# Optimization experiments

Hardware: AMD Instinct MI355X
Metric: run time of the kernel (lower is better)

## Reference

```python
import jax, jax.numpy as jnp
import numpy as np

SIDE = 32
N_NODES = SIDE * SIDE          # n_nodes = 1024
WIDTH = 128
IN_DIM = 128
T_DIM = 2
U_DIM = 1
BATCH = 8
MSG_STEPS = int(np.sqrt(N_NODES))  # 32
LN_EPS = 1e-5


def _create_grid():
    # matches GEN.create_grid for t_dim == 2
    pos = np.array([[i / (SIDE - 1), j / (SIDE - 1)]
                    for i in range(SIDE) for j in range(SIDE)], dtype=np.float32)
    edges = []
    for i in range(1, SIDE):
        for j in range(1, SIDE):
            a = SIDE * i + j
            b = SIDE * (i - 1) + j
            c = SIDE * i + (j - 1)
            edges += [[a, b], [b, a], [c, a], [a, c]]
    edge_index = np.array(edges, dtype=np.int64).T  # [2, E]
    return pos, edge_index


def setup_inputs() -> dict:
    key = jax.random.key(0)
    ks = jax.random.split(key, 16)
    node_pos_np, edge_index_np = _create_grid()

    def lin(k, fan_in, fan_out):
        kw, kb = jax.random.split(k)
        bound = 1.0 / np.sqrt(fan_in)
        W = jax.random.uniform(kw, (fan_in, fan_out), jnp.float32, -bound, bound)
        b = jax.random.uniform(kb, (fan_out,), jnp.float32, -bound, bound)
        return W, b

    We1, be1 = lin(ks[0], IN_DIM, WIDTH)
    We2, be2 = lin(ks[1], WIDTH, WIDTH)
    We3, be3 = lin(ks[2], WIDTH, WIDTH)
    Wg, bg = lin(ks[3], WIDTH + T_DIM, WIDTH)
    Wd1, bd1 = lin(ks[4], WIDTH + T_DIM, WIDTH)
    Wd2, bd2 = lin(ks[5], WIDTH, WIDTH)
    Wd3, bd3 = lin(ks[6], WIDTH, U_DIM)

    return {
        'X1': jax.random.uniform(ks[7], (BATCH, IN_DIM + T_DIM), jnp.float32),
        'node_pos': jnp.asarray(node_pos_np),
        'edge_index': jnp.asarray(edge_index_np),
        'We1': We1, 'be1': be1, 'We2': We2, 'be2': be2, 'We3': We3, 'be3': be3,
        'Wg': Wg, 'bg': bg,
        'gamma': jnp.ones((WIDTH,), jnp.float32),
        'beta': jnp.zeros((WIDTH,), jnp.float32),
        'Wd1': Wd1, 'bd1': bd1, 'Wd2': Wd2, 'bd2': bd2, 'Wd3': Wd3, 'bd3': bd3,
    }


def _gen_forward(X1, node_pos, edge_index, We1, be1, We2, be2, We3, be3,
                 Wg, bg, gamma, beta, Wd1, bd1, Wd2, bd2, Wd3, bd3):
    s, t = X1[:, :-T_DIM], X1[:, -T_DIM:]

    # encoder MLP: Linear-ReLU-Linear-ReLU-Linear
    h = jax.nn.relu(s @ We1 + be1)
    h = jax.nn.relu(h @ We2 + be2)
    enc = h @ We3 + be3                                   # [B, W]

    # per-sample graph construction: softmax over node distance to origin
    # (identical for every sample), node_features = weight @ enc[i][None,:]
    d0 = jnp.sqrt(jnp.sum(node_pos ** 2, axis=1, keepdims=True))  # [N,1]
    w0 = jax.nn.softmax(-d0, axis=0)                              # [N,1]
    x = w0[None, :, :] * enc[:, None, :]                          # [B,N,W]

    # GCNConv normalization with added self-loops (symmetric norm)
    row, col = edge_index[0], edge_index[1]
    deg = jnp.ones((N_NODES,), x.dtype).at[col].add(1.0)
    dinv = deg ** -0.5
    enorm = dinv[row] * dinv[col]   # edge norm
    snorm = dinv * dinv             # self-loop norm
    posb = jnp.broadcast_to(node_pos[None], (x.shape[0], N_NODES, T_DIM))

    def step(xc, _):
        xin = jnp.concatenate([posb, xc], axis=-1)        # [B,N,W+2]
        xw = xin @ Wg                                     # [B,N,W]
        msgs = enorm[None, :, None] * xw[:, row, :]       # [B,E,W]
        agg = (snorm[None, :, None] * xw).at[:, col, :].add(msgs) + bg
        xn = xc + agg
        mu = jnp.mean(xn, axis=-1, keepdims=True)
        var = jnp.var(xn, axis=-1, keepdims=True)
        xn = (xn - mu) * jax.lax.rsqrt(var + LN_EPS) * gamma + beta
        return xn, None

    x, _ = jax.lax.scan(step, x, None, length=MSG_STEPS)  # [B,N,W]

    # readout: softmax over node distance to query point t
    dist = jnp.sqrt(jnp.sum((node_pos[None] - t[:, None, :]) ** 2,
                            axis=2, keepdims=True))       # [B,N,1]
    wt = jax.nn.softmax(-dist, axis=1)                    # [B,N,1]
    hidden = jnp.einsum('bnk,bnw->bw', wt, x)             # [B,W]
    hidden = jnp.concatenate([hidden, t], axis=1)

    h = jax.nn.relu(hidden @ Wd1 + bd1)
    h = jax.nn.relu(h @ Wd2 + bd2)
    y = (h @ Wd3 + bd3).squeeze()                         # [B] (u_dim == 1)
    return y


def reference(X1, node_pos, edge_index, We1, be1, We2, be2, We3, be3,
              Wg, bg, gamma, beta, Wd1, bd1, Wd2, bd2, Wd3, bd3):
    return _gen_forward(X1, node_pos, edge_index, We1, be1, We2, be2, We3, be3,
                        Wg, bg, gamma, beta, Wd1, bd1, Wd2, bd2, Wd3, bd3)
```

## Files before the change

kernel.cpp:

```cpp
#include <hip/hip_runtime.h>

#define NODES 1024
#define WD    128
#define NSTEPS 32
#define LNEPS 1e-5f

typedef __bf16 bf16x8 __attribute__((ext_vector_type(8)));
typedef float  f32x4  __attribute__((ext_vector_type(4)));
typedef int    i32x4  __attribute__((ext_vector_type(4)));

__device__ __forceinline__ f32x4 mfma16(i32x4 a, i32x4 b, f32x4 c) {
  return __builtin_amdgcn_mfma_f32_16x16x32_bf16(
      __builtin_bit_cast(bf16x8, a), __builtin_bit_cast(bf16x8, b), c, 0, 0, 0);
}

__device__ __forceinline__ unsigned short f2bf(float f) {
  union { float f; unsigned u; } v; v.f = f;
  unsigned r = v.u + 0x7FFF + ((v.u >> 16) & 1);
  return (unsigned short)(r >> 16);
}
__device__ __forceinline__ float bf2f(unsigned short h) {
  union { unsigned u; float f; } v; v.u = ((unsigned)h) << 16;
  return v.f;
}

__device__ __forceinline__ float dinv_of(int n) {
  const int i = n >> 5, j = n & 31;
  int cnt = 1;
  cnt += (i >= 1 && j >= 1) ? 1 : 0;
  cnt += (i <= 30 && j >= 1) ? 1 : 0;
  cnt += (i >= 1 && j >= 1) ? 1 : 0;
  cnt += (i >= 1 && j <= 30) ? 1 : 0;
  return 1.f / sqrtf((float)cnt);
}

__device__ __forceinline__ void lay512(const float* __restrict__ W,
                                       const float* __restrict__ bias,
                                       const float* __restrict__ src,
                                       float* __restrict__ dst, int tid,
                                       bool relu_) {
  const int c = tid & 127;
  const int b0 = tid >> 7;
  float a0 = bias ? bias[c] : 0.f;
  float a1 = a0;
#pragma unroll 8
  for (int k = 0; k < WD; k++) {
    const float wv = W[k * WD + c];
    a0 += src[b0 * WD + k] * wv;
    a1 += src[(b0 + 4) * WD + k] * wv;
  }
  dst[b0 * WD + c] = relu_ ? fmaxf(a0, 0.f) : a0;
  dst[(b0 + 4) * WD + c] = relu_ ? fmaxf(a1, 0.f) : a1;
  __syncthreads();
}

__global__ __launch_bounds__(512) void init_kernel(
    const float* __restrict__ X1, const float* __restrict__ pos,
    const float* __restrict__ We1, const float* __restrict__ be1,
    const float* __restrict__ We2, const float* __restrict__ be2,
    const float* __restrict__ We3, const float* __restrict__ be3,
    const float* __restrict__ Wg, const float* __restrict__ bg,
    float* __restrict__ X, float* __restrict__ XW0, float* __restrict__ Q,
    int* __restrict__ Bpk) {
  __shared__ float ioA[1024];
  __shared__ float ioB[1024];
  __shared__ float red[512];
  const int tid = threadIdx.x;
  const int v0 = blockIdx.x * 4;
  const float* W2 = Wg + 2 * WD;

  for (int i = tid; i < 1024; i += 512) ioA[i] = X1[(i >> 7) * 130 + (i & 127)];
  __syncthreads();
  lay512(We1, be1, ioA, ioB, tid, true);
  lay512(We2, be2, ioB, ioA, tid, true);
  lay512(We3, be3, ioA, ioB, tid, false);
  lay512(W2, nullptr, ioB, ioA, tid, false);

  {
    float es = 0.f;
#pragma unroll
    for (int r = 0; r < 2; r++) {
      const int n = tid + 512 * r;
      const float px = pos[2 * n], py = pos[2 * n + 1];
      es += expf(-sqrtf(px * px + py * py));
    }
    red[tid] = es;
  }
  __syncthreads();
  for (int s = 256; s > 0; s >>= 1) {
    if (tid < s) red[tid] += red[tid + s];
    __syncthreads();
  }
  const float w0sum = red[0];

  {
    const int lr = tid >> 4, cq = tid & 15, c0 = cq * 8;
    const int b = lr >> 2, nl = lr & 3, v = v0 + nl;
    const int grow = (b << 10) + v;
    const float pxv = pos[2 * v], pyv = pos[2 * v + 1];
    const float w0v = expf(-sqrtf(pxv * pxv + pyv * pyv)) / w0sum;
#pragma unroll
    for (int q4 = 0; q4 < 2; q4++) {
      const float4 e = *(const float4*)(ioB + b * WD + c0 + 4 * q4);
      const float4 e2 = *(const float4*)(ioA + b * WD + c0 + 4 * q4);
      *(float4*)(X + (size_t)grow * WD + c0 + 4 * q4) =
          make_float4(w0v * e.x, w0v * e.y, w0v * e.z, w0v * e.w);
      *(float4*)(XW0 + (size_t)grow * WD + c0 + 4 * q4) =
          make_float4(w0v * e2.x, w0v * e2.y, w0v * e2.z, w0v * e2.w);
    }
  }
  {
    const int vq = v0 + (tid >> 7);
    const int cc = tid & 127;
    const float dv = dinv_of(vq);
    const float dvv = dv * dv;
    const int iv = vq >> 5, jv = vq & 31;
    float cx = dvv * pos[2 * vq], cy = dvv * pos[2 * vq + 1];
    const bool ex[4] = {(iv >= 1) && (jv >= 1), (iv <= 30) && (jv >= 1),
                        (iv >= 1) && (jv >= 1), (iv >= 1) && (jv <= 30)};
    const int du[4] = {-32, 32, -1, 1};
#pragma unroll
    for (int e = 0; e < 4; e++) {
      if (ex[e]) {
        const int u = vq + du[e];
        const float w = dinv_of(u) * dv;
        cx += w * pos[2 * u];
        cy += w * pos[2 * u + 1];
      }
    }
    Q[vq * WD + cc] = bg[cc] + cx * Wg[cc] + cy * Wg[WD + cc];
  }
  if (tid < 64) {
    const int e = blockIdx.x * 64 + tid;
    const int nt = e >> 11, l = (e >> 5) & 63, half = (e >> 4) & 1;
    const int kt = (e >> 2) & 3, d = e & 3;
    const int k0 = 32 * kt + ((l >> 4) << 3) + 2 * d;
    const int n = 16 * nt + (l & 15);
    const float w0_ = W2[k0 * WD + n];
    const float w1_ = W2[(k0 + 1) * WD + n];
    const unsigned short h0 = f2bf(w0_), h1 = f2bf(w1_);
    int val;
    if (half == 0) {
      val = (int)h0 | ((int)h1 << 16);
    } else {
      val = (int)f2bf(w0_ - bf2f(h0)) | ((int)f2bf(w1_ - bf2f(h1)) << 16);
    }
    Bpk[e] = val;
  }
}

__global__ __launch_bounds__(512) void step_kernel(
    float* __restrict__ X, const float* __restrict__ XWin,
    float* __restrict__ XWout, const int* __restrict__ Bpk,
    const float* __restrict__ Q, const float* __restrict__ gamma,
    const float* __restrict__ beta, const int mode) {
  __shared__ int Ah[32 * 68];
  __shared__ int Al[32 * 68];
  const int tid = threadIdx.x;
  const int v0 = blockIdx.x * 4;
  const int wv = tid >> 6, l = tid & 63;

  i32x4 bh[4], bl[4];
  if (mode) {
    const int lb0 = (wv * 64 + l) * 32;
#pragma unroll
    for (int kt = 0; kt < 4; kt++) {
      bh[kt] = *(const i32x4*)(Bpk + lb0 + kt * 4);
      bl[kt] = *(const i32x4*)(Bpk + lb0 + 16 + kt * 4);
    }
  }

  const int lr = tid >> 4, cq = tid & 15, c0 = cq * 8;
  const int b = lr >> 2, nl = lr & 3, v = v0 + nl;
  const int grow = (b << 10) + v;
  const float dv = dinv_of(v);
  const float dvv = dv * dv;
  const int iv = v >> 5, jv = v & 31;
  const bool ex[4] = {(iv >= 1) && (jv >= 1), (iv <= 30) && (jv >= 1),
                      (iv >= 1) && (jv >= 1), (iv >= 1) && (jv <= 30)};
  const int du[4] = {-32, 32, -1, 1};

  float y[8];
  {
    const float* xr = X + (size_t)grow * WD + c0;
    const float* qr = Q + v * WD + c0;
    const float* wr = XWin + (size_t)grow * WD + c0;
#pragma unroll
    for (int q4 = 0; q4 < 2; q4++) {
      const float4 a = *(const float4*)(xr + 4 * q4);
      const float4 qq = *(const float4*)(qr + 4 * q4);
      const float4 w = *(const float4*)(wr + 4 * q4);
      y[4 * q4 + 0] = a.x + qq.x + dvv * w.x;
      y[4 * q4 + 1] = a.y + qq.y + dvv * w.y;
      y[4 * q4 + 2] = a.z + qq.z + dvv * w.z;
      y[4 * q4 + 3] = a.w + qq.w + dvv * w.w;
    }
  }
#pragma unroll
  for (int e = 0; e < 4; e++) {
    const int u = ex[e] ? v + du[e] : v;
    const float w = ex[e] ? dinv_of(u) * dv : 0.f;
    const float* nr = XWin + (size_t)((b << 10) + u) * WD + c0;
#pragma unroll
    for (int q4 = 0; q4 < 2; q4++) {
      const float4 t = *(const float4*)(nr + 4 * q4);
      y[4 * q4 + 0] += w * t.x;
      y[4 * q4 + 1] += w * t.y;
      y[4 * q4 + 2] += w * t.z;
      y[4 * q4 + 3] += w * t.w;
    }
  }
  float s1 = 0.f, s2 = 0.f;
#pragma unroll
  for (int q = 0; q < 8; q++) { s1 += y[q]; s2 += y[q] * y[q]; }
#pragma unroll
  for (int m = 1; m < 16; m <<= 1) {
    s1 += __shfl_xor(s1, m);
    s2 += __shfl_xor(s2, m);
  }
  const float mu = s1 * (1.f / 128.f);
  const float var = s2 * (1.f / 128.f) - mu * mu;
  const float rs = 1.f / sqrtf(var + LNEPS);
  {
    const float* g4 = gamma + c0;
    const float* b4 = beta + c0;
    float* xo = X + (size_t)grow * WD + c0;
    float xn[8];
#pragma unroll
    for (int q = 0; q < 8; q++) xn[q] = (y[q] - mu) * rs * g4[q] + b4[q];
    *(float4*)(xo) = make_float4(xn[0], xn[1], xn[2], xn[3]);
    *(float4*)(xo + 4) = make_float4(xn[4], xn[5], xn[6], xn[7]);
    if (mode) {
      int hw[4], lw[4];
#pragma unroll
      for (int d = 0; d < 4; d++) {
        const unsigned short ha = f2bf(xn[2 * d]);
        const unsigned short hb = f2bf(xn[2 * d + 1]);
        hw[d] = (int)ha | ((int)hb << 16);
        lw[d] = (int)f2bf(xn[2 * d] - bf2f(ha)) |
                ((int)f2bf(xn[2 * d + 1] - bf2f(hb)) << 16);
      }
      const int abase = lr * 68 + cq * 4;
      *(i32x4*)(Ah + abase) = i32x4{hw[0], hw[1], hw[2], hw[3]};
      *(i32x4*)(Al + abase) = i32x4{lw[0], lw[1], lw[2], lw[3]};
    }
  }

  if (mode) {
    __syncthreads();
    const int g4 = (l >> 4) << 2;
    const int mrow0 = (l & 15) * 68;
    const int mrow1 = mrow0 + 16 * 68;
    f32x4 acc[2] = {};
#pragma unroll
    for (int kt = 0; kt < 4; kt++) {
      const int off = 16 * kt + g4;
      const i32x4 ah0 = *(const i32x4*)(Ah + mrow0 + off);
      const i32x4 ah1 = *(const i32x4*)(Ah + mrow1 + off);
      const i32x4 al0 = *(const i32x4*)(Al + mrow0 + off);
      const i32x4 al1 = *(const i32x4*)(Al + mrow1 + off);
      acc[0] = mfma16(ah0, bh[kt], acc[0]);
      acc[1] = mfma16(ah1, bh[kt], acc[1]);
      acc[0] = mfma16(ah0, bl[kt], acc[0]);
      acc[1] = mfma16(ah1, bl[kt], acc[1]);
      acc[0] = mfma16(al0, bh[kt], acc[0]);
      acc[1] = mfma16(al1, bh[kt], acc[1]);
    }
    const int colb = 16 * wv + (l & 15);
    const int rbase = (l >> 4) << 2;
#pragma unroll
    for (int mt = 0; mt < 2; mt++)
#pragma unroll
      for (int r = 0; r < 4; r++) {
        const int lrr = 16 * mt + rbase + r;
        const int gr = ((lrr >> 2) << 10) + v0 + (lrr & 3);
        XWout[(size_t)gr * WD + colb] = acc[mt][r];
      }
  }
}

__global__ __launch_bounds__(1024) void hiddec_kernel(
    const float* __restrict__ pos, const float* __restrict__ X1,
    const float* __restrict__ Xf, const float* __restrict__ Wd1,
    const float* __restrict__ bd1, const float* __restrict__ Wd2,
    const float* __restrict__ bd2, const float* __restrict__ Wd3,
    const float* __restrict__ bd3, float* __restrict__ out) {
  __shared__ float wsh[NODES];
  __shared__ float red[16];
  __shared__ float asum[8][WD];
  __shared__ float hid[132];
  __shared__ float hh[WD];
  const int b = blockIdx.x;
  const int n = threadIdx.x;
  const float tx = X1[b * 130 + 128], ty = X1[b * 130 + 129];
  const float px = pos[2 * n] - tx, py = pos[2 * n + 1] - ty;
  const float e = expf(-sqrtf(px * px + py * py));
  float s = e;
#pragma unroll
  for (int m = 32; m >= 1; m >>= 1) s += __shfl_xor(s, m);
  if ((n & 63) == 0) red[n >> 6] = s;
  __syncthreads();
  float tot = 0.f;
#pragma unroll
  for (int w = 0; w < 16; w++) tot += red[w];
  wsh[n] = e / tot;
  __syncthreads();
  const int c = n & 127, g = n >> 7;
  {
    const float* xp = Xf + ((size_t)b * NODES + g * 128) * WD + c;
    const float* wp = wsh + g * 128;
    float a = 0.f;
#pragma unroll 4
    for (int it = 0; it < 128; it++) a += wp[it] * xp[it * WD];
    asum[g][c] = a;
  }
  __syncthreads();
  if (g == 0) {
    float t2 = asum[0][c];
#pragma unroll
    for (int gg = 1; gg < 8; gg++) t2 += asum[gg][c];
    hid[c] = t2;
  }
  if (n == 0) { hid[128] = tx; hid[129] = ty; }
  __syncthreads();
  float a1v = 0.f;
  if (n < 128) {
    a1v = bd1[n];
    for (int k = 0; k < 130; k++) a1v += hid[k] * Wd1[k * WD + n];
  }
  __syncthreads();
  if (n < 128) hh[n] = fmaxf(a1v, 0.f);
  __syncthreads();
  float p = 0.f;
  if (n < 128) {
    float a2 = bd2[n];
#pragma unroll 8
    for (int k = 0; k < WD; k++) a2 += hh[k] * Wd2[k * WD + n];
    p = fmaxf(a2, 0.f) * Wd3[n];
  }
#pragma unroll
  for (int m = 32; m >= 1; m >>= 1) p += __shfl_xor(p, m);
  if ((n & 63) == 0) red[n >> 6] = p;
  __syncthreads();
  if (n == 0) out[b] = red[0] + red[1] + bd3[0];
}

extern "C" void kernel_launch(void* const* d_in, const int* in_sizes, int n_in,
                              void* d_out, int out_size, void* d_ws,
                              size_t ws_size, hipStream_t stream) {
  const float* X1 = (const float*)d_in[0];
  const float* pos = (const float*)d_in[1];
  const float* We1 = (const float*)d_in[3];
  const float* be1 = (const float*)d_in[4];
  const float* We2 = (const float*)d_in[5];
  const float* be2 = (const float*)d_in[6];
  const float* We3 = (const float*)d_in[7];
  const float* be3 = (const float*)d_in[8];
  const float* Wg = (const float*)d_in[9];
  const float* bg = (const float*)d_in[10];
  const float* gamma = (const float*)d_in[11];
  const float* beta = (const float*)d_in[12];
  const float* Wd1 = (const float*)d_in[13];
  const float* bd1 = (const float*)d_in[14];
  const float* Wd2 = (const float*)d_in[15];
  const float* bd2 = (const float*)d_in[16];
  const float* Wd3 = (const float*)d_in[17];
  const float* bd3 = (const float*)d_in[18];
  float* out = (float*)d_out;
  float* f = (float*)d_ws;

  float* Q = f;
  int* Bpk = (int*)(f + 131072);
  float* X = f + 147456;
  float* XWa = f + 1196032;
  float* XWb = f + 2244608;

  init_kernel<<<256, 512, 0, stream>>>(X1, pos, We1, be1, We2, be2, We3, be3,
                                       Wg, bg, X, XWa, Q, Bpk);
  for (int t = 0; t < NSTEPS; t++) {
    const float* xin = (t & 1) ? XWb : XWa;
    float* xout = (t & 1) ? XWa : XWb;
    step_kernel<<<256, 512, 0, stream>>>(X, xin, xout, Bpk, Q, gamma, beta,
                                         (t < NSTEPS - 1) ? 1 : 0);
  }
  hiddec_kernel<<<8, 1024, 0, stream>>>(pos, X1, X, Wd1, bd1, Wd2, bd2, Wd3,
                                        bd3, out);
  (void)in_sizes;
  (void)n_in;
  (void)out_size;
  (void)ws_size;
}
```

Measured before the change: 263.8 us.

## Fuse two message-passing steps per launch with halo recomputation

Each launch now does two graph steps. The first step is recomputed over a halo of neighbour nodes (4 own plus 10 halo nodes per block), and its XW projection is kept in shared memory for the second step. This halves the number of step kernel launches and removes one global round trip of X and XW per pair of steps. In exchange it adds redundant halo compute and MFMA work (7 row tiles instead of 2), uses much more shared memory per block, and now ping-pongs X between two buffers.

New measurement: 490.6 us. 86.0% more time.

```diff
diff --git a/kernel.cpp b/kernel.cpp
--- a/kernel.cpp
+++ b/kernel.cpp
@@ -149,19 +149,22 @@
   }
 }
 
-__global__ __launch_bounds__(512) void step_kernel(
-    float* __restrict__ X, const float* __restrict__ XWin,
-    float* __restrict__ XWout, const int* __restrict__ Bpk,
-    const float* __restrict__ Q, const float* __restrict__ gamma,
-    const float* __restrict__ beta, const int mode) {
-  __shared__ int Ah[32 * 68];
-  __shared__ int Al[32 * 68];
+__global__ __launch_bounds__(512) void step2_kernel(
+    const float* __restrict__ Xin, float* __restrict__ Xout,
+    const float* __restrict__ XWin, float* __restrict__ XWout,
+    const int* __restrict__ Bpk, const float* __restrict__ Q,
+    const float* __restrict__ gamma, const float* __restrict__ beta,
+    const int last) {
+  __shared__ int R1[15232];
+  __shared__ float X1own[32 * 132];
+  __shared__ int R3[4352];
   const int tid = threadIdx.x;
   const int v0 = blockIdx.x * 4;
   const int wv = tid >> 6, l = tid & 63;
+  const int i0 = v0 >> 5, j0 = v0 & 31;
 
   i32x4 bh[4], bl[4];
-  if (mode) {
+  {
     const int lb0 = (wv * 64 + l) * 32;
 #pragma unroll
     for (int kt = 0; kt < 4; kt++) {
@@ -170,67 +173,182 @@
     }
   }
 
-  const int lr = tid >> 4, cq = tid & 15, c0 = cq * 8;
-  const int b = lr >> 2, nl = lr & 3, v = v0 + nl;
-  const int grow = (b << 10) + v;
-  const float dv = dinv_of(v);
-  const float dvv = dv * dv;
-  const int iv = v >> 5, jv = v & 31;
-  const bool ex[4] = {(iv >= 1) && (jv >= 1), (iv <= 30) && (jv >= 1),
-                      (iv >= 1) && (jv >= 1), (iv >= 1) && (jv <= 30)};
-  const int du[4] = {-32, 32, -1, 1};
-
-  float y[8];
-  {
-    const float* xr = X + (size_t)grow * WD + c0;
-    const float* qr = Q + v * WD + c0;
-    const float* wr = XWin + (size_t)grow * WD + c0;
-#pragma unroll
-    for (int q4 = 0; q4 < 2; q4++) {
-      const float4 a = *(const float4*)(xr + 4 * q4);
-      const float4 qq = *(const float4*)(qr + 4 * q4);
-      const float4 w = *(const float4*)(wr + 4 * q4);
-      y[4 * q4 + 0] = a.x + qq.x + dvv * w.x;
-      y[4 * q4 + 1] = a.y + qq.y + dvv * w.y;
-      y[4 * q4 + 2] = a.z + qq.z + dvv * w.z;
-      y[4 * q4 + 3] = a.w + qq.w + dvv * w.w;
-    }
-  }
-#pragma unroll
-  for (int e = 0; e < 4; e++) {
-    const int u = ex[e] ? v + du[e] : v;
-    const float w = ex[e] ? dinv_of(u) * dv : 0.f;
-    const float* nr = XWin + (size_t)((b << 10) + u) * WD + c0;
-#pragma unroll
-    for (int q4 = 0; q4 < 2; q4++) {
-      const float4 t = *(const float4*)(nr + 4 * q4);
-      y[4 * q4 + 0] += w * t.x;
-      y[4 * q4 + 1] += w * t.y;
-      y[4 * q4 + 2] += w * t.z;
-      y[4 * q4 + 3] += w * t.w;
-    }
-  }
-  float s1 = 0.f, s2 = 0.f;
-#pragma unroll
-  for (int q = 0; q < 8; q++) { s1 += y[q]; s2 += y[q] * y[q]; }
-#pragma unroll
-  for (int m = 1; m < 16; m <<= 1) {
-    s1 += __shfl_xor(s1, m);
-    s2 += __shfl_xor(s2, m);
-  }
-  const float mu = s1 * (1.f / 128.f);
-  const float var = s2 * (1.f / 128.f) - mu * mu;
-  const float rs = 1.f / sqrtf(var + LNEPS);
-  {
-    const float* g4 = gamma + c0;
-    const float* b4 = beta + c0;
-    float* xo = X + (size_t)grow * WD + c0;
+  if (tid < 448) {
+    const int hrow = tid >> 2;
+    const int ck = tid & 3;
+    const int c0 = ck * 32;
+    const int h = hrow >> 3, b = hrow & 7;
+    int u;
+    bool valid;
+    if (h < 4)       { u = v0 + h;            valid = true; }
+    else if (h == 4) { u = v0 - 1;            valid = (j0 >= 1); }
+    else if (h == 5) { u = v0 + 4;            valid = (j0 + 4 <= 31); }
+    else if (h < 10) { u = v0 - 32 + (h - 6); valid = (i0 >= 1); }
+    else             { u = v0 + 32 + (h - 10); valid = (i0 <= 30); }
+    if (!valid) u = v0;
+    const float du_ = dinv_of(u);
+    const float duu = du_ * du_;
+    const int iu = u >> 5, ju = u & 31;
+    const bool exu[4] = {iu >= 1 && ju >= 1, iu <= 30 && ju >= 1,
+                         iu >= 1 && ju >= 1, iu >= 1 && ju <= 31 - 1};
+    const int dd[4] = {-32, 32, -1, 1};
+    float y[32];
+    {
+      const float* xr = Xin + (size_t)((b << 10) + u) * WD + c0;
+      const float* qr = Q + u * WD + c0;
+      const float* wr = XWin + (size_t)((b << 10) + u) * WD + c0;
+#pragma unroll
+      for (int q4 = 0; q4 < 8; q4++) {
+        const float4 a = *(const float4*)(xr + 4 * q4);
+        const float4 qq = *(const float4*)(qr + 4 * q4);
+        const float4 w = *(const float4*)(wr + 4 * q4);
+        y[4 * q4 + 0] = a.x + qq.x + duu * w.x;
+        y[4 * q4 + 1] = a.y + qq.y + duu * w.y;
+        y[4 * q4 + 2] = a.z + qq.z + duu * w.z;
+        y[4 * q4 + 3] = a.w + qq.w + duu * w.w;
+      }
+    }
+#pragma unroll
+    for (int e = 0; e < 4; e++) {
+      const int un = exu[e] ? u + dd[e] : u;
+      const float w = exu[e] ? dinv_of(un) * du_ : 0.f;
+      const float* nr = XWin + (size_t)((b << 10) + un) * WD + c0;
+#pragma unroll
+      for (int q4 = 0; q4 < 8; q4++) {
+        const float4 t = *(const float4*)(nr + 4 * q4);
+        y[4 * q4 + 0] += w * t.x;
+        y[4 * q4 + 1] += w * t.y;
+        y[4 * q4 + 2] += w * t.z;
+        y[4 * q4 + 3] += w * t.w;
+      }
+    }
+    float s1 = 0.f, s2 = 0.f;
+#pragma unroll
+    for (int q = 0; q < 32; q++) { s1 += y[q]; s2 += y[q] * y[q]; }
+#pragma unroll
+    for (int m = 1; m < 4; m <<= 1) {
+      s1 += __shfl_xor(s1, m);
+      s2 += __shfl_xor(s2, m);
+    }
+    const float mu = s1 * (1.f / 128.f);
+    const float var = s2 * (1.f / 128.f) - mu * mu;
+    const float rs = 1.f / sqrtf(var + LNEPS);
+    const float* gp = gamma + c0;
+    const float* bp = beta + c0;
+    int hw[16], lw[16];
+#pragma unroll
+    for (int d = 0; d < 16; d++) {
+      const float xa = (y[2 * d] - mu) * rs * gp[2 * d] + bp[2 * d];
+      const float xb = (y[2 * d + 1] - mu) * rs * gp[2 * d + 1] + bp[2 * d + 1];
+      if (hrow < 32)
+        *(float2*)(X1own + hrow * 132 + c0 + 2 * d) = make_float2(xa, xb);
+      const unsigned short ha = f2bf(xa), hb = f2bf(xb);
+      hw[d] = (int)ha | ((int)hb << 16);
+      lw[d] = (int)f2bf(xa - bf2f(ha)) | ((int)f2bf(xb - bf2f(hb)) << 16);
+    }
+    const int ab = hrow * 68 + ck * 16;
+#pragma unroll
+    for (int g = 0; g < 4; g++) {
+      *(i32x4*)(R1 + ab + 4 * g) = i32x4{hw[4*g], hw[4*g+1], hw[4*g+2], hw[4*g+3]};
+      *(i32x4*)(R1 + 7616 + ab + 4 * g) =
+          i32x4{lw[4*g], lw[4*g+1], lw[4*g+2], lw[4*g+3]};
+    }
+  }
+  __syncthreads();
+
+  f32x4 acc1[7] = {};
+  {
+    const int g4 = (l >> 4) << 2;
+    const int mr = l & 15;
+#pragma unroll
+    for (int kt = 0; kt < 4; kt++) {
+      const int off = 16 * kt + g4;
+#pragma unroll
+      for (int mt = 0; mt < 7; mt++) {
+        const int rb = (mt * 16 + mr) * 68 + off;
+        const i32x4 ah = *(const i32x4*)(R1 + rb);
+        const i32x4 al = *(const i32x4*)(R1 + 7616 + rb);
+        acc1[mt] = mfma16(ah, bh[kt], acc1[mt]);
+        acc1[mt] = mfma16(ah, bl[kt], acc1[mt]);
+        acc1[mt] = mfma16(al, bh[kt], acc1[mt]);
+      }
+    }
+  }
+  __syncthreads();
+  {
+    float* XW1 = (float*)R1;
+    const int colb = 16 * wv + (l & 15);
+    const int rbase = (l >> 4) << 2;
+#pragma unroll
+    for (int mt = 0; mt < 7; mt++)
+#pragma unroll
+      for (int r = 0; r < 4; r++)
+        XW1[(mt * 16 + rbase + r) * 132 + colb] = acc1[mt][r];
+  }
+  __syncthreads();
+
+  const float* XW1c = (const float*)R1;
+  {
+    const int lr = tid >> 4, cq = tid & 15, c0b = cq * 8;
+    const int bb = lr >> 2, nl = lr & 3;
+    const int v = v0 + nl;
+    const float dv = dinv_of(v);
+    const float dvv = dv * dv;
+    const int iv = v >> 5, jv = v & 31;
+    const bool exv[4] = {iv >= 1 && jv >= 1, iv <= 30 && jv >= 1,
+                         iv >= 1 && jv >= 1, iv >= 1 && jv <= 30};
+    const int du[4] = {-32, 32, -1, 1};
+    const int hn[4] = {6 + nl, 10 + nl, (nl == 0) ? 4 : nl - 1,
+                       (nl == 3) ? 5 : nl + 1};
+    float y[8];
+    {
+      const float* s = XW1c + (nl * 8 + bb) * 132 + c0b;
+      const float* xo = X1own + (nl * 8 + bb) * 132 + c0b;
+      const float* qr = Q + v * WD + c0b;
+#pragma unroll
+      for (int q4 = 0; q4 < 2; q4++) {
+        const float4 a = *(const float4*)(xo + 4 * q4);
+        const float4 qq = *(const float4*)(qr + 4 * q4);
+        const float4 w = *(const float4*)(s + 4 * q4);
+        y[4 * q4 + 0] = a.x + qq.x + dvv * w.x;
+        y[4 * q4 + 1] = a.y + qq.y + dvv * w.y;
+        y[4 * q4 + 2] = a.z + qq.z + dvv * w.z;
+        y[4 * q4 + 3] = a.w + qq.w + dvv * w.w;
+      }
+    }
+#pragma unroll
+    for (int e = 0; e < 4; e++) {
+      const float w = exv[e] ? dinv_of(v + du[e]) * dv : 0.f;
+      const float* nr = XW1c + (hn[e] * 8 + bb) * 132 + c0b;
+#pragma unroll
+      for (int q4 = 0; q4 < 2; q4++) {
+        const float4 t = *(const float4*)(nr + 4 * q4);
+        y[4 * q4 + 0] += w * t.x;
+        y[4 * q4 + 1] += w * t.y;
+        y[4 * q4 + 2] += w * t.z;
+        y[4 * q4 + 3] += w * t.w;
+      }
+    }
+    float s1 = 0.f, s2 = 0.f;
+#pragma unroll
+    for (int q = 0; q < 8; q++) { s1 += y[q]; s2 += y[q] * y[q]; }
+#pragma unroll
+    for (int m = 1; m < 16; m <<= 1) {
+      s1 += __shfl_xor(s1, m);
+      s2 += __shfl_xor(s2, m);
+    }
+    const float mu = s1 * (1.f / 128.f);
+    const float var = s2 * (1.f / 128.f) - mu * mu;
+    const float rs = 1.f / sqrtf(var + LNEPS);
+    const float* gp = gamma + c0b;
+    const float* bp = beta + c0b;
     float xn[8];
 #pragma unroll
-    for (int q = 0; q < 8; q++) xn[q] = (y[q] - mu) * rs * g4[q] + b4[q];
+    for (int q = 0; q < 8; q++) xn[q] = (y[q] - mu) * rs * gp[q] + bp[q];
+    float* xo = Xout + (size_t)((bb << 10) + v) * WD + c0b;
     *(float4*)(xo) = make_float4(xn[0], xn[1], xn[2], xn[3]);
     *(float4*)(xo + 4) = make_float4(xn[4], xn[5], xn[6], xn[7]);
-    if (mode) {
+    if (!last) {
       int hw[4], lw[4];
 #pragma unroll
       for (int d = 0; d < 4; d++) {
@@ -240,31 +358,31 @@
         lw[d] = (int)f2bf(xn[2 * d] - bf2f(ha)) |
                 ((int)f2bf(xn[2 * d + 1] - bf2f(hb)) << 16);
       }
-      const int abase = lr * 68 + cq * 4;
-      *(i32x4*)(Ah + abase) = i32x4{hw[0], hw[1], hw[2], hw[3]};
-      *(i32x4*)(Al + abase) = i32x4{lw[0], lw[1], lw[2], lw[3]};
-    }
-  }
-
-  if (mode) {
+      const int ab = lr * 68 + cq * 4;
+      *(i32x4*)(R3 + ab) = i32x4{hw[0], hw[1], hw[2], hw[3]};
+      *(i32x4*)(R3 + 2176 + ab) = i32x4{lw[0], lw[1], lw[2], lw[3]};
+    }
+  }
+
+  if (!last) {
     __syncthreads();
+    f32x4 acc2[2] = {};
     const int g4 = (l >> 4) << 2;
-    const int mrow0 = (l & 15) * 68;
-    const int mrow1 = mrow0 + 16 * 68;
-    f32x4 acc[2] = {};
+    const int mr0 = (l & 15) * 68;
+    const int mr1 = (16 + (l & 15)) * 68;
 #pragma unroll
     for (int kt = 0; kt < 4; kt++) {
       const int off = 16 * kt + g4;
-      const i32x4 ah0 = *(const i32x4*)(Ah + mrow0 + off);
-      const i32x4 ah1 = *(const i32x4*)(Ah + mrow1 + off);
-      const i32x4 al0 = *(const i32x4*)(Al + mrow0 + off);
-      const i32x4 al1 = *(const i32x4*)(Al + mrow1 + off);
-      acc[0] = mfma16(ah0, bh[kt], acc[0]);
-      acc[1] = mfma16(ah1, bh[kt], acc[1]);
-      acc[0] = mfma16(ah0, bl[kt], acc[0]);
-      acc[1] = mfma16(ah1, bl[kt], acc[1]);
-      acc[0] = mfma16(al0, bh[kt], acc[0]);
-      acc[1] = mfma16(al1, bh[kt], acc[1]);
+      const i32x4 ah0 = *(const i32x4*)(R3 + mr0 + off);
+      const i32x4 ah1 = *(const i32x4*)(R3 + mr1 + off);
+      const i32x4 al0 = *(const i32x4*)(R3 + 2176 + mr0 + off);
+      const i32x4 al1 = *(const i32x4*)(R3 + 2176 + mr1 + off);
+      acc2[0] = mfma16(ah0, bh[kt], acc2[0]);
+      acc2[1] = mfma16(ah1, bh[kt], acc2[1]);
+      acc2[0] = mfma16(ah0, bl[kt], acc2[0]);
+      acc2[1] = mfma16(ah1, bl[kt], acc2[1]);
+      acc2[0] = mfma16(al0, bh[kt], acc2[0]);
+      acc2[1] = mfma16(al1, bh[kt], acc2[1]);
     }
     const int colb = 16 * wv + (l & 15);
     const int rbase = (l >> 4) << 2;
@@ -274,7 +392,7 @@
       for (int r = 0; r < 4; r++) {
         const int lrr = 16 * mt + rbase + r;
         const int gr = ((lrr >> 2) << 10) + v0 + (lrr & 3);
-        XWout[(size_t)gr * WD + colb] = acc[mt][r];
+        XWout[(size_t)gr * WD + colb] = acc2[mt][r];
       }
   }
 }
@@ -371,19 +489,23 @@
 
   float* Q = f;
   int* Bpk = (int*)(f + 131072);
-  float* X = f + 147456;
-  float* XWa = f + 1196032;
-  float* XWb = f + 2244608;
+  float* Xa = f + 147456;
+  float* Xb = f + 1196032;
+  float* XWa = f + 2244608;
+  float* XWb = f + 3293184;
 
   init_kernel<<<256, 512, 0, stream>>>(X1, pos, We1, be1, We2, be2, We3, be3,
-                                       Wg, bg, X, XWa, Q, Bpk);
-  for (int t = 0; t < NSTEPS; t++) {
-    const float* xin = (t & 1) ? XWb : XWa;
-    float* xout = (t & 1) ? XWa : XWb;
-    step_kernel<<<256, 512, 0, stream>>>(X, xin, xout, Bpk, Q, gamma, beta,
-                                         (t < NSTEPS - 1) ? 1 : 0);
-  }
-  hiddec_kernel<<<8, 1024, 0, stream>>>(pos, X1, X, Wd1, bd1, Wd2, bd2, Wd3,
+                                       Wg, bg, Xa, XWa, Q, Bpk);
+  for (int p = 0; p < NSTEPS / 2; p++) {
+    const float* xin = (p & 1) ? Xb : Xa;
+    float* xout = (p & 1) ? Xa : Xb;
+    const float* xwin = (p & 1) ? XWb : XWa;
+    float* xwout = (p & 1) ? XWa : XWb;
+    step2_kernel<<<256, 512, 0, stream>>>(xin, xout, xwin, xwout, Bpk, Q,
+                                          gamma, beta,
+                                          (p == NSTEPS / 2 - 1) ? 1 : 0);
+  }
+  hiddec_kernel<<<8, 1024, 0, stream>>>(pos, X1, Xa, Wd1, bd1, Wd2, bd2, Wd3,
                                         bd3, out);
   (void)in_sizes;
   (void)n_in;
```

## Recompute halo XW product per step instead of storing XW globally

Applied to the files above, without the earlier changes.

Each step kernel now loads X for its 4 nodes plus a 14-node halo of neighbours, converts them to split bf16 in shared memory, and computes X·W with MFMA locally before aggregation and layernorm. This replaces the previous scheme, which wrote XW to a global ping-pong buffer and read neighbour XW rows, and it removes the XW0 computation from init. The intent is to cut global traffic, since only X now round-trips through global memory. In exchange each block does 3.5x more MFMA work on the halo rows and the kernel uses about 60 KB of shared memory per block, which may reduce occupancy.

Result: slower. 309.5 us (+17.3%).

```diff
diff --git a/kernel.cpp b/kernel.cpp
--- a/kernel.cpp
+++ b/kernel.cpp
@@ -60,8 +60,7 @@
     const float* __restrict__ We2, const float* __restrict__ be2,
     const float* __restrict__ We3, const float* __restrict__ be3,
     const float* __restrict__ Wg, const float* __restrict__ bg,
-    float* __restrict__ X, float* __restrict__ XW0, float* __restrict__ Q,
-    int* __restrict__ Bpk) {
+    float* __restrict__ X, float* __restrict__ Q, int* __restrict__ Bpk) {
   __shared__ float ioA[1024];
   __shared__ float ioB[1024];
   __shared__ float red[512];
@@ -74,7 +73,6 @@
   lay512(We1, be1, ioA, ioB, tid, true);
   lay512(We2, be2, ioB, ioA, tid, true);
   lay512(We3, be3, ioA, ioB, tid, false);
-  lay512(W2, nullptr, ioB, ioA, tid, false);
 
   {
     float es = 0.f;
@@ -102,11 +100,8 @@
 #pragma unroll
     for (int q4 = 0; q4 < 2; q4++) {
       const float4 e = *(const float4*)(ioB + b * WD + c0 + 4 * q4);
-      const float4 e2 = *(const float4*)(ioA + b * WD + c0 + 4 * q4);
       *(float4*)(X + (size_t)grow * WD + c0 + 4 * q4) =
           make_float4(w0v * e.x, w0v * e.y, w0v * e.z, w0v * e.w);
-      *(float4*)(XW0 + (size_t)grow * WD + c0 + 4 * q4) =
-          make_float4(w0v * e2.x, w0v * e2.y, w0v * e2.z, w0v * e2.w);
     }
   }
   {
@@ -149,19 +144,18 @@
   }
 }
 
-__global__ __launch_bounds__(512) void step_kernel(
-    float* __restrict__ X, const float* __restrict__ XWin,
-    float* __restrict__ XWout, const int* __restrict__ Bpk,
-    const float* __restrict__ Q, const float* __restrict__ gamma,
-    const float* __restrict__ beta, const int mode) {
-  __shared__ int Ah[32 * 68];
-  __shared__ int Al[32 * 68];
+__global__ __launch_bounds__(512) void stepH_kernel(
+    const float* __restrict__ Xin, float* __restrict__ Xout,
+    const int* __restrict__ Bpk, const float* __restrict__ Q,
+    const float* __restrict__ gamma, const float* __restrict__ beta) {
+  __shared__ int R1[15232];
   const int tid = threadIdx.x;
   const int v0 = blockIdx.x * 4;
   const int wv = tid >> 6, l = tid & 63;
+  const int i0 = v0 >> 5, j0 = v0 & 31;
 
   i32x4 bh[4], bl[4];
-  if (mode) {
+  {
     const int lb0 = (wv * 64 + l) * 32;
 #pragma unroll
     for (int kt = 0; kt < 4; kt++) {
@@ -171,111 +165,131 @@
   }
 
   const int lr = tid >> 4, cq = tid & 15, c0 = cq * 8;
-  const int b = lr >> 2, nl = lr & 3, v = v0 + nl;
-  const int grow = (b << 10) + v;
-  const float dv = dinv_of(v);
-  const float dvv = dv * dv;
-  const int iv = v >> 5, jv = v & 31;
-  const bool ex[4] = {(iv >= 1) && (jv >= 1), (iv <= 30) && (jv >= 1),
-                      (iv >= 1) && (jv >= 1), (iv >= 1) && (jv <= 30)};
-  const int du[4] = {-32, 32, -1, 1};
-
-  float y[8];
-  {
-    const float* xr = X + (size_t)grow * WD + c0;
-    const float* qr = Q + v * WD + c0;
-    const float* wr = XWin + (size_t)grow * WD + c0;
-#pragma unroll
-    for (int q4 = 0; q4 < 2; q4++) {
-      const float4 a = *(const float4*)(xr + 4 * q4);
-      const float4 qq = *(const float4*)(qr + 4 * q4);
-      const float4 w = *(const float4*)(wr + 4 * q4);
-      y[4 * q4 + 0] = a.x + qq.x + dvv * w.x;
-      y[4 * q4 + 1] = a.y + qq.y + dvv * w.y;
-      y[4 * q4 + 2] = a.z + qq.z + dvv * w.z;
-      y[4 * q4 + 3] = a.w + qq.w + dvv * w.w;
-    }
-  }
-#pragma unroll
-  for (int e = 0; e < 4; e++) {
-    const int u = ex[e] ? v + du[e] : v;
-    const float w = ex[e] ? dinv_of(u) * dv : 0.f;
-    const float* nr = XWin + (size_t)((b << 10) + u) * WD + c0;
-#pragma unroll
-    for (int q4 = 0; q4 < 2; q4++) {
-      const float4 t = *(const float4*)(nr + 4 * q4);
-      y[4 * q4 + 0] += w * t.x;
-      y[4 * q4 + 1] += w * t.y;
-      y[4 * q4 + 2] += w * t.z;
-      y[4 * q4 + 3] += w * t.w;
-    }
-  }
-  float s1 = 0.f, s2 = 0.f;
-#pragma unroll
-  for (int q = 0; q < 8; q++) { s1 += y[q]; s2 += y[q] * y[q]; }
-#pragma unroll
-  for (int m = 1; m < 16; m <<= 1) {
-    s1 += __shfl_xor(s1, m);
-    s2 += __shfl_xor(s2, m);
-  }
-  const float mu = s1 * (1.f / 128.f);
-  const float var = s2 * (1.f / 128.f) - mu * mu;
-  const float rs = 1.f / sqrtf(var + LNEPS);
-  {
-    const float* g4 = gamma + c0;
-    const float* b4 = beta + c0;
-    float* xo = X + (size_t)grow * WD + c0;
+  const int bb = lr >> 2, nl = lr & 3, v = v0 + nl;
+  const float* xop = Xin + (size_t)((bb << 10) + v) * WD + c0;
+  const float* qp = Q + v * WD + c0;
+  const float4 xo0 = *(const float4*)(xop);
+  const float4 xo1 = *(const float4*)(xop + 4);
+  const float4 qq0 = *(const float4*)(qp);
+  const float4 qq1 = *(const float4*)(qp + 4);
+
+  if (tid < 448) {
+    const int h = tid >> 5, m = tid & 31;
+    int u;
+    bool valid;
+    if (h < 4)       { u = v0 + h;             valid = true; }
+    else if (h == 4) { u = v0 - 1;             valid = (j0 >= 1); }
+    else if (h == 5) { u = v0 + 4;             valid = (j0 + 4 <= 31); }
+    else if (h < 10) { u = v0 - 32 + (h - 6);  valid = (i0 >= 1); }
+    else             { u = v0 + 32 + (h - 10); valid = (i0 <= 30); }
+    if (!valid) u = v0;
+#pragma unroll
+    for (int j = 0; j < 8; j++) {
+      const float4 xv =
+          *(const float4*)(Xin + (size_t)((j << 10) + u) * WD + 4 * m);
+      const unsigned short h0 = f2bf(xv.x), h1 = f2bf(xv.y);
+      const unsigned short h2 = f2bf(xv.z), h3 = f2bf(xv.w);
+      int2 hi, lo;
+      hi.x = (int)h0 | ((int)h1 << 16);
+      hi.y = (int)h2 | ((int)h3 << 16);
+      lo.x = (int)f2bf(xv.x - bf2f(h0)) | ((int)f2bf(xv.y - bf2f(h1)) << 16);
+      lo.y = (int)f2bf(xv.z - bf2f(h2)) | ((int)f2bf(xv.w - bf2f(h3)) << 16);
+      const int ab = (h * 8 + j) * 68 + 2 * m;
+      *(int2*)(R1 + ab) = hi;
+      *(int2*)(R1 + 7616 + ab) = lo;
+    }
+  }
+  __syncthreads();
+
+  f32x4 acc[7] = {};
+  {
+    const int g4 = (l >> 4) << 2;
+    const int mr = l & 15;
+#pragma unroll
+    for (int kt = 0; kt < 4; kt++) {
+      const int off = 16 * kt + g4;
+#pragma unroll
+      for (int mt = 0; mt < 7; mt++) {
+        const int rb = (mt * 16 + mr) * 68 + off;
+        const i32x4 ah = *(const i32x4*)(R1 + rb);
+        const i32x4 al = *(const i32x4*)(R1 + 7616 + rb);
+        acc[mt] = mfma16(ah, bh[kt], acc[mt]);
+        acc[mt] = mfma16(ah, bl[kt], acc[mt]);
+        acc[mt] = mfma16(al, bh[kt], acc[mt]);
+      }
+    }
+  }
+  __syncthreads();
+  {
+    float* XW1 = (float*)R1;
+    const int colb = 16 * wv + (l & 15);
+    const int rbase = (l >> 4) << 2;
+#pragma unroll
+    for (int mt = 0; mt < 7; mt++)
+#pragma unroll
+      for (int r = 0; r < 4; r++)
+        XW1[(mt * 16 + rbase + r) * 132 + colb] = acc[mt][r];
+  }
+  __syncthreads();
+
+  {
+    const float* XW1c = (const float*)R1;
+    const float dv = dinv_of(v);
+    const float dvv = dv * dv;
+    const int iv = v >> 5, jv = v & 31;
+    const bool exv[4] = {iv >= 1 && jv >= 1, iv <= 30 && jv >= 1,
+                         iv >= 1 && jv >= 1, iv >= 1 && jv <= 30};
+    const int du[4] = {-32, 32, -1, 1};
+    const int hn[4] = {6 + nl, 10 + nl, (nl == 0) ? 4 : nl - 1,
+                       (nl == 3) ? 5 : nl + 1};
+    float y[8];
+    {
+      const float* s = XW1c + (nl * 8 + bb) * 132 + c0;
+      const float4 w0v = *(const float4*)(s);
+      const float4 w1v = *(const float4*)(s + 4);
+      y[0] = xo0.x + qq0.x + dvv * w0v.x;
+      y[1] = xo0.y + qq0.y + dvv * w0v.y;
+      y[2] = xo0.z + qq0.z + dvv * w0v.z;
+      y[3] = xo0.w + qq0.w + dvv * w0v.w;
+      y[4] = xo1.x + qq1.x + dvv * w1v.x;
+      y[5] = xo1.y + qq1.y + dvv * w1v.y;
+      y[6] = xo1.z + qq1.z + dvv * w1v.z;
+      y[7] = xo1.w + qq1.w + dvv * w1v.w;
+    }
+#pragma unroll
+    for (int e = 0; e < 4; e++) {
+      const float w = exv[e] ? dinv_of(v + du[e]) * dv : 0.f;
+      const float* nr = XW1c + (hn[e] * 8 + bb) * 132 + c0;
+      const float4 t0 = *(const float4*)(nr);
+      const float4 t1 = *(const float4*)(nr + 4);
+      y[0] += w * t0.x;
+      y[1] += w * t0.y;
+      y[2] += w * t0.z;
+      y[3] += w * t0.w;
+      y[4] += w * t1.x;
+      y[5] += w * t1.y;
+      y[6] += w * t1.z;
+      y[7] += w * t1.w;
+    }
+    float s1 = 0.f, s2 = 0.f;
+#pragma unroll
+    for (int q = 0; q < 8; q++) { s1 += y[q]; s2 += y[q] * y[q]; }
+#pragma unroll
+    for (int m = 1; m < 16; m <<= 1) {
+      s1 += __shfl_xor(s1, m);
+      s2 += __shfl_xor(s2, m);
+    }
+    const float mu = s1 * (1.f / 128.f);
+    const float var = s2 * (1.f / 128.f) - mu * mu;
+    const float rs = 1.f / sqrtf(var + LNEPS);
+    const float* gp = gamma + c0;
+    const float* bp = beta + c0;
     float xn[8];
 #pragma unroll
-    for (int q = 0; q < 8; q++) xn[q] = (y[q] - mu) * rs * g4[q] + b4[q];
+    for (int q = 0; q < 8; q++) xn[q] = (y[q] - mu) * rs * gp[q] + bp[q];
+    float* xo = Xout + (size_t)((bb << 10) + v) * WD + c0;
     *(float4*)(xo) = make_float4(xn[0], xn[1], xn[2], xn[3]);
     *(float4*)(xo + 4) = make_float4(xn[4], xn[5], xn[6], xn[7]);
-    if (mode) {
-      int hw[4], lw[4];
-#pragma unroll
-      for (int d = 0; d < 4; d++) {
-        const unsigned short ha = f2bf(xn[2 * d]);
-        const unsigned short hb = f2bf(xn[2 * d + 1]);
-        hw[d] = (int)ha | ((int)hb << 16);
-        lw[d] = (int)f2bf(xn[2 * d] - bf2f(ha)) |
-                ((int)f2bf(xn[2 * d + 1] - bf2f(hb)) << 16);
-      }
-      const int abase = lr * 68 + cq * 4;
-      *(i32x4*)(Ah + abase) = i32x4{hw[0], hw[1], hw[2], hw[3]};
-      *(i32x4*)(Al + abase) = i32x4{lw[0], lw[1], lw[2], lw[3]};
-    }
-  }
-
-  if (mode) {
-    __syncthreads();
-    const int g4 = (l >> 4) << 2;
-    const int mrow0 = (l & 15) * 68;
-    const int mrow1 = mrow0 + 16 * 68;
-    f32x4 acc[2] = {};
-#pragma unroll
-    for (int kt = 0; kt < 4; kt++) {
-      const int off = 16 * kt + g4;
-      const i32x4 ah0 = *(const i32x4*)(Ah + mrow0 + off);
-      const i32x4 ah1 = *(const i32x4*)(Ah + mrow1 + off);
-      const i32x4 al0 = *(const i32x4*)(Al + mrow0 + off);
-      const i32x4 al1 = *(const i32x4*)(Al + mrow1 + off);
-      acc[0] = mfma16(ah0, bh[kt], acc[0]);
-      acc[1] = mfma16(ah1, bh[kt], acc[1]);
-      acc[0] = mfma16(ah0, bl[kt], acc[0]);
-      acc[1] = mfma16(ah1, bl[kt], acc[1]);
-      acc[0] = mfma16(al0, bh[kt], acc[0]);
-      acc[1] = mfma16(al1, bh[kt], acc[1]);
-    }
-    const int colb = 16 * wv + (l & 15);
-    const int rbase = (l >> 4) << 2;
-#pragma unroll
-    for (int mt = 0; mt < 2; mt++)
-#pragma unroll
-      for (int r = 0; r < 4; r++) {
-        const int lrr = 16 * mt + rbase + r;
-        const int gr = ((lrr >> 2) << 10) + v0 + (lrr & 3);
-        XWout[(size_t)gr * WD + colb] = acc[mt][r];
-      }
   }
 }
 
@@ -371,19 +385,17 @@
 
   float* Q = f;
   int* Bpk = (int*)(f + 131072);
-  float* X = f + 147456;
-  float* XWa = f + 1196032;
-  float* XWb = f + 2244608;
+  float* Xa = f + 147456;
+  float* Xb = f + 1196032;
 
   init_kernel<<<256, 512, 0, stream>>>(X1, pos, We1, be1, We2, be2, We3, be3,
-                                       Wg, bg, X, XWa, Q, Bpk);
+                                       Wg, bg, Xa, Q, Bpk);
   for (int t = 0; t < NSTEPS; t++) {
-    const float* xin = (t & 1) ? XWb : XWa;
-    float* xout = (t & 1) ? XWa : XWb;
-    step_kernel<<<256, 512, 0, stream>>>(X, xin, xout, Bpk, Q, gamma, beta,
-                                         (t < NSTEPS - 1) ? 1 : 0);
-  }
-  hiddec_kernel<<<8, 1024, 0, stream>>>(pos, X1, X, Wd1, bd1, Wd2, bd2, Wd3,
+    const float* xin = (t & 1) ? Xb : Xa;
+    float* xout = (t & 1) ? Xa : Xb;
+    stepH_kernel<<<256, 512, 0, stream>>>(xin, xout, Bpk, Q, gamma, beta);
+  }
+  hiddec_kernel<<<8, 1024, 0, stream>>>(pos, X1, Xa, Wd1, bd1, Wd2, bd2, Wd3,
                                         bd3, out);
   (void)in_sizes;
   (void)n_in;
```

## Split step kernel into 512 blocks of 256 threads, two nodes each

Applied to the files above, without the earlier changes.

Each step block now handles 2 nodes instead of 4 (16 rows across 8 batches), launching 512 blocks of 256 threads so more of the GPU's compute units get work. Each wave now computes two 16-column output tiles, holding two sets of B fragments in registers, and reuses each A fragment across both tiles. The trade-off is that the packed weight matrix is loaded by twice as many blocks, and register pressure per wave goes up.

Result: slower. 344.5 us (+30.6%).

```diff
diff --git a/kernel.cpp b/kernel.cpp
--- a/kernel.cpp
+++ b/kernel.cpp
@@ -149,30 +149,33 @@
   }
 }
 
-__global__ __launch_bounds__(512) void step_kernel(
+__global__ __launch_bounds__(256, 2) void step_kernel(
     float* __restrict__ X, const float* __restrict__ XWin,
     float* __restrict__ XWout, const int* __restrict__ Bpk,
     const float* __restrict__ Q, const float* __restrict__ gamma,
     const float* __restrict__ beta, const int mode) {
-  __shared__ int Ah[32 * 68];
-  __shared__ int Al[32 * 68];
+  __shared__ int Ah[16 * 68];
+  __shared__ int Al[16 * 68];
   const int tid = threadIdx.x;
-  const int v0 = blockIdx.x * 4;
+  const int v0 = blockIdx.x * 2;
   const int wv = tid >> 6, l = tid & 63;
 
-  i32x4 bh[4], bl[4];
+  i32x4 bh[2][4], bl[2][4];
   if (mode) {
-    const int lb0 = (wv * 64 + l) * 32;
-#pragma unroll
-    for (int kt = 0; kt < 4; kt++) {
-      bh[kt] = *(const i32x4*)(Bpk + lb0 + kt * 4);
-      bl[kt] = *(const i32x4*)(Bpk + lb0 + 16 + kt * 4);
+#pragma unroll
+    for (int ntl = 0; ntl < 2; ntl++) {
+      const int lb0 = ((2 * wv + ntl) * 64 + l) * 32;
+#pragma unroll
+      for (int kt = 0; kt < 4; kt++) {
+        bh[ntl][kt] = *(const i32x4*)(Bpk + lb0 + kt * 4);
+        bl[ntl][kt] = *(const i32x4*)(Bpk + lb0 + 16 + kt * 4);
+      }
     }
   }
 
   const int lr = tid >> 4, cq = tid & 15, c0 = cq * 8;
-  const int b = lr >> 2, nl = lr & 3, v = v0 + nl;
-  const int grow = (b << 10) + v;
+  const int bb = lr >> 1, nl = lr & 1, v = v0 + nl;
+  const int grow = (bb << 10) + v;
   const float dv = dinv_of(v);
   const float dvv = dv * dv;
   const int iv = v >> 5, jv = v & 31;
@@ -200,7 +203,7 @@
   for (int e = 0; e < 4; e++) {
     const int u = ex[e] ? v + du[e] : v;
     const float w = ex[e] ? dinv_of(u) * dv : 0.f;
-    const float* nr = XWin + (size_t)((b << 10) + u) * WD + c0;
+    const float* nr = XWin + (size_t)((bb << 10) + u) * WD + c0;
 #pragma unroll
     for (int q4 = 0; q4 < 2; q4++) {
       const float4 t = *(const float4*)(nr + 4 * q4);
@@ -249,33 +252,31 @@
   if (mode) {
     __syncthreads();
     const int g4 = (l >> 4) << 2;
-    const int mrow0 = (l & 15) * 68;
-    const int mrow1 = mrow0 + 16 * 68;
+    const int mrow = (l & 15) * 68;
     f32x4 acc[2] = {};
 #pragma unroll
     for (int kt = 0; kt < 4; kt++) {
       const int off = 16 * kt + g4;
-      const i32x4 ah0 = *(const i32x4*)(Ah + mrow0 + off);
-      const i32x4 ah1 = *(const i32x4*)(Ah + mrow1 + off);
-      const i32x4 al0 = *(const i32x4*)(Al + mrow0 + off);
-      const i32x4 al1 = *(const i32x4*)(Al + mrow1 + off);
-      acc[0] = mfma16(ah0, bh[kt], acc[0]);
-      acc[1] = mfma16(ah1, bh[kt], acc[1]);
-      acc[0] = mfma16(ah0, bl[kt], acc[0]);
-      acc[1] = mfma16(ah1, bl[kt], acc[1]);
-      acc[0] = mfma16(al0, bh[kt], acc[0]);
-      acc[1] = mfma16(al1, bh[kt], acc[1]);
-    }
-    const int colb = 16 * wv + (l & 15);
+      const i32x4 ah = *(const i32x4*)(Ah + mrow + off);
+      const i32x4 al = *(const i32x4*)(Al + mrow + off);
+#pragma unroll
+      for (int ntl = 0; ntl < 2; ntl++) {
+        acc[ntl] = mfma16(ah, bh[ntl][kt], acc[ntl]);
+        acc[ntl] = mfma16(ah, bl[ntl][kt], acc[ntl]);
+        acc[ntl] = mfma16(al, bh[ntl][kt], acc[ntl]);
+      }
+    }
     const int rbase = (l >> 4) << 2;
 #pragma unroll
-    for (int mt = 0; mt < 2; mt++)
+    for (int ntl = 0; ntl < 2; ntl++) {
+      const int colb = 16 * (2 * wv + ntl) + (l & 15);
 #pragma unroll
       for (int r = 0; r < 4; r++) {
-        const int lrr = 16 * mt + rbase + r;
-        const int gr = ((lrr >> 2) << 10) + v0 + (lrr & 3);
-        XWout[(size_t)gr * WD + colb] = acc[mt][r];
-      }
+        const int lrr = rbase + r;
+        const int gr = ((lrr >> 1) << 10) + v0 + (lrr & 1);
+        XWout[(size_t)gr * WD + colb] = acc[ntl][r];
+      }
+    }
   }
 }
 
@@ -380,7 +381,8 @@
   for (int t = 0; t < NSTEPS; t++) {
     const float* xin = (t & 1) ? XWb : XWa;
     float* xout = (t & 1) ? XWa : XWb;
-    step_kernel<<<256, 512, 0, stream>>>(X, xin, xout, Bpk, Q, gamma, beta,
+    step_kernel<<<512, 256, 0, stream>>>(X, (const float*)xin, xout, Bpk, Q,
+                                         gamma, beta,
                                          (t < NSTEPS - 1) ? 1 : 0);
   }
   hiddec_kernel<<<8, 1024, 0, stream>>>(pos, X1, X, Wd1, bd1, Wd2, bd2, Wd3,
```
